# Kernel optimization log

Hardware: AMD Instinct MI355X
Metric: run time of the kernel (lower is better)

Reference implementation:

```python
import jax, jax.numpy as jnp
import numpy as np
from functools import partial

THRESH = 0.5   # similarity_threshold
EPS = 1e-8     # F.cosine_similarity eps


def setup_inputs() -> dict:
    key = jax.random.key(0)
    # uniform positive vectors -> pairwise cosine ~0.75 > threshold, so merges actually occur
    embeddings = jax.random.uniform(key, (8192, 512), dtype=jnp.float32)
    return {"embeddings": embeddings}


@partial(jax.jit, static_argnums=())
def _greedy_match(embs):
    """One merge round. Returns (partner[i] or -1, consumed-as-j flag per i).
    Faithful to the original greedy: scan i in order; i picks argmax-sim j>i among
    not-yet-merged with sim >= threshold; both get marked merged."""
    n = embs.shape[0]
    norms = jnp.maximum(jnp.linalg.norm(embs, axis=-1), EPS)
    sim = (embs @ embs.T) / (norms[:, None] * norms[None, :])  # [n, n]
    idx = jnp.arange(n)

    def step(merged, xs):
        i, row = xs
        was_consumed = merged[i]
        valid = (~merged) & (idx > i)
        scores = jnp.where(valid, row, -jnp.inf)
        j = jnp.argmax(scores)
        ok = (~was_consumed) & (scores[j] >= THRESH)
        merged = merged.at[i].set(was_consumed | ok)
        merged = merged.at[j].set(merged[j] | ok)
        return merged, (jnp.where(ok, j, -1), was_consumed)

    _, (partners, consumed) = jax.lax.scan(step, jnp.zeros(n, bool), (idx, sim))
    return partners, consumed


def reference(embeddings):
    embs = embeddings
    # outer while-loop mirrors the module: iterate rounds until no merge or n<=1
    while embs.shape[0] > 1:
        partners, consumed = _greedy_match(embs)
        partners_np = np.asarray(partners)
        if not (partners_np >= 0).any():  # merge_occurred == False
            break
        safe = jnp.maximum(partners, 0)
        # fuse_embeddings: clamp(v1 + v2, max=1.0); non-leaders keep their row
        fused = jnp.where((partners >= 0)[:, None],
                          jnp.minimum(embs + embs[safe], 1.0), embs)
        survivors = np.where(~np.asarray(consumed))[0]  # rows not consumed as a j
        embs = fused[survivors]
    return embs
```

## Files before the change

### kernel.cpp

```cpp
#include <hip/hip_runtime.h>
#include <math.h>

#define D 512
#define THRESH 0.5f
#define NMAX 8192
#define TOPK 64
#define INFI 0x7fffffff

typedef short bhalf8 __attribute__((ext_vector_type(8)));
typedef float f32x4 __attribute__((ext_vector_type(4)));

__device__ __forceinline__ unsigned long long rdl64(unsigned long long x, int l) {
    unsigned lo = (unsigned)__builtin_amdgcn_readlane((int)(unsigned)(x & 0xffffffffull), l);
    unsigned hi = (unsigned)__builtin_amdgcn_readlane((int)(unsigned)(x >> 32), l);
    return ((unsigned long long)hi << 32) | lo;
}

__global__ void k_init(int* dn, int n) { *dn = n; }

__global__ void k_prep(const float* __restrict__ E, float* __restrict__ norms,
                       unsigned short* __restrict__ H, const int* __restrict__ dn) {
    int n = *dn;
    int row = blockIdx.x;
    if (row >= n) return;
    int t = threadIdx.x;
    float4 v = ((const float4*)(E + (size_t)row * D))[t];
    float s = v.x * v.x + v.y * v.y + v.z * v.z + v.w * v.w;
    #pragma unroll
    for (int o = 32; o > 0; o >>= 1) s += __shfl_down(s, o, 64);
    __shared__ float ls[2];
    if ((t & 63) == 0) ls[t >> 6] = s;
    float f[4] = {v.x, v.y, v.z, v.w};
    unsigned short r[4];
    #pragma unroll
    for (int u = 0; u < 4; ++u) {
        unsigned int b = __float_as_uint(f[u]);
        r[u] = (unsigned short)((b + 0x7FFFu + ((b >> 16) & 1u)) >> 16);
    }
    uint2 packed;
    packed.x = (unsigned)r[0] | ((unsigned)r[1] << 16);
    packed.y = (unsigned)r[2] | ((unsigned)r[3] << 16);
    *(uint2*)(H + (size_t)row * D + t * 4) = packed;
    __syncthreads();
    if (t == 0) norms[row] = fmaxf(sqrtf(ls[0] + ls[1]), 1e-8f);
}

#define LDSTRIDE 72
__global__ void __launch_bounds__(256) k_mfma_sim(
    const unsigned short* __restrict__ H, const float* __restrict__ norms,
    float* __restrict__ sim, int tile_start, int TR, int simStride,
    const int* __restrict__ dn)
{
    int n = *dn;
    if (tile_start >= n) return;
    int row0 = tile_start + blockIdx.y * 128;
    int col0 = blockIdx.x * 128;
    if (row0 >= n || col0 >= n) return;
    if (col0 + 128 <= row0 + 1) return;

    __shared__ unsigned short As[128 * LDSTRIDE];
    __shared__ unsigned short Bs[128 * LDSTRIDE];
    int tid = threadIdx.x;
    int lane = tid & 63;
    int wave = tid >> 6;
    int wr = wave >> 1;
    int wc = wave & 1;
    int krow = lane & 15;
    int kgrp = (lane >> 4) * 8;

    f32x4 acc[4][4];
    #pragma unroll
    for (int m = 0; m < 4; ++m)
        #pragma unroll
        for (int t = 0; t < 4; ++t)
            acc[m][t] = (f32x4){0.f, 0.f, 0.f, 0.f};

    for (int k0 = 0; k0 < D; k0 += 64) {
        #pragma unroll
        for (int it = 0; it < 4; ++it) {
            int c  = tid + it * 256;
            int rr = c >> 3;
            int cc = c & 7;
            uint4 va = make_uint4(0, 0, 0, 0);
            int gra = row0 + rr;
            if (gra < n) va = *(const uint4*)(H + (size_t)gra * D + k0 + cc * 8);
            *(uint4*)&As[rr * LDSTRIDE + cc * 8] = va;
            uint4 vb = make_uint4(0, 0, 0, 0);
            int grb = col0 + rr;
            if (grb < n) vb = *(const uint4*)(H + (size_t)grb * D + k0 + cc * 8);
            *(uint4*)&Bs[rr * LDSTRIDE + cc * 8] = vb;
        }
        __syncthreads();
        #pragma unroll
        for (int kk = 0; kk < 64; kk += 32) {
            bhalf8 a[4], b[4];
            #pragma unroll
            for (int m = 0; m < 4; ++m)
                a[m] = *(const bhalf8*)&As[(wr * 64 + m * 16 + krow) * LDSTRIDE + kk + kgrp];
            #pragma unroll
            for (int t = 0; t < 4; ++t)
                b[t] = *(const bhalf8*)&Bs[(wc * 64 + t * 16 + krow) * LDSTRIDE + kk + kgrp];
            #pragma unroll
            for (int m = 0; m < 4; ++m)
                #pragma unroll
                for (int t = 0; t < 4; ++t)
                    acc[m][t] = __builtin_amdgcn_mfma_f32_16x16x32_bf16(a[m], b[t], acc[m][t], 0, 0, 0);
        }
        __syncthreads();
    }

    int fcol = lane & 15;
    int frow = (lane >> 4) * 4;
    #pragma unroll
    for (int m = 0; m < 4; ++m) {
        #pragma unroll
        for (int t = 0; t < 4; ++t) {
            #pragma unroll
            for (int v = 0; v < 4; ++v) {
                int gr = row0 + wr * 64 + m * 16 + frow + v;
                int gc = col0 + wc * 64 + t * 16 + fcol;
                if (gr < n && gc < n)
                    sim[(size_t)(gr - tile_start) * simStride + gc] =
                        acc[m][t][v] / (norms[gr] * norms[gc]);
            }
        }
    }
}

__global__ void __launch_bounds__(64) k_topk(
    const float* __restrict__ sim, int tile_start, int TR, int simStride,
    uint2* __restrict__ tkP, int* __restrict__ needFix,
    const int* __restrict__ dn)
{
    int n = *dn;
    int r = blockIdx.x;
    int i = tile_start + r;
    if (r >= TR || i >= n) return;
    int lane = threadIdx.x;
    const float* srow = sim + (size_t)r * simStride;

    float v[8]; int id[8];
    #pragma unroll
    for (int u = 0; u < 8; ++u) { v[u] = -INFINITY; id[u] = INFI; }
    float ovV = -INFINITY; int ovI = INFI;

    for (int j = i + 1 + lane; j < n; j += 64) {
        float x = srow[j];
        if (x > v[7] || (x == v[7] && j < id[7])) {
            if (v[7] > ovV || (v[7] == ovV && id[7] < ovI)) { ovV = v[7]; ovI = id[7]; }
            int p = 7;
            #pragma unroll
            for (int u = 6; u >= 0; --u) {
                bool mv = (x > v[u]) || (x == v[u] && j < id[u]);
                if (mv) { v[u + 1] = v[u]; id[u + 1] = id[u]; p = u; }
            }
            v[p] = x; id[p] = j;
        } else {
            if (x > ovV || (x == ovV && j < ovI)) { ovV = x; ovI = j; }
        }
    }

    int pos = 0;
    float myV = -INFINITY; int myI = INFI;
    for (int k = 0; k < TOPK; ++k) {
        float hv = (pos < 8) ? v[pos] : -INFINITY;
        int   hi = (pos < 8) ? id[pos] : INFI;
        float bv = hv; int bi = hi;
        #pragma unroll
        for (int o = 1; o < 64; o <<= 1) {
            float xv = __shfl_xor(bv, o, 64);
            int   xi = __shfl_xor(bi, o, 64);
            if (xv > bv || (xv == bv && xi < bi)) { bv = xv; bi = xi; }
        }
        if (pos < 8 && hv == bv && hi == bi) pos++;
        if (k == lane) { myV = bv; myI = bi; }
    }
    tkP[(size_t)i * TOPK + lane] = make_uint2(__float_as_uint(myV), (unsigned)myI);

    float v64 = __shfl(myV, 63, 64);
    int   i64 = __shfl(myI, 63, 64);
    float oV = ovV; int oI = ovI;
    #pragma unroll
    for (int o = 1; o < 64; o <<= 1) {
        float xv = __shfl_xor(oV, o, 64);
        int   xi = __shfl_xor(oI, o, 64);
        if (xv > oV || (xv == oV && xi < oI)) { oV = xv; oI = xi; }
    }
    int bad = (oV > v64) || (oV == v64 && oI < i64);
    if (lane == 0) needFix[i] = bad;
}

__global__ void __launch_bounds__(64) k_topkfix(
    const float* __restrict__ sim, int tile_start, int TR, int simStride,
    uint2* __restrict__ tkP, const int* __restrict__ needFix,
    const int* __restrict__ dn)
{
    int n = *dn;
    int r = blockIdx.x;
    int i = tile_start + r;
    if (r >= TR || i >= n) return;
    if (!needFix[i]) return;
    int lane = threadIdx.x;
    __shared__ float lv[64][TOPK];
    __shared__ int   li[64][TOPK];
    for (int u = 0; u < TOPK; ++u) { lv[lane][u] = -INFINITY; li[lane][u] = INFI; }
    const float* srow = sim + (size_t)r * simStride;
    for (int j = i + 1 + lane; j < n; j += 64) {
        float x = srow[j];
        float wv = lv[lane][TOPK - 1]; int wi = li[lane][TOPK - 1];
        if (x > wv || (x == wv && j < wi)) {
            int p = TOPK - 1;
            for (int u = TOPK - 2; u >= 0; --u) {
                float uv = lv[lane][u]; int ui = li[lane][u];
                if (x > uv || (x == uv && j < ui)) { lv[lane][u + 1] = uv; li[lane][u + 1] = ui; p = u; }
                else break;
            }
            lv[lane][p] = x; li[lane][p] = j;
        }
    }
    int pos = 0;
    float myV = -INFINITY; int myI = INFI;
    for (int k = 0; k < TOPK; ++k) {
        float hv = (pos < TOPK) ? lv[lane][pos] : -INFINITY;
        int   hi = (pos < TOPK) ? li[lane][pos] : INFI;
        float bv = hv; int bi = hi;
        #pragma unroll
        for (int o = 1; o < 64; o <<= 1) {
            float xv = __shfl_xor(bv, o, 64);
            int   xi = __shfl_xor(bi, o, 64);
            if (xv > bv || (xv == bv && xi < bi)) { bv = xv; bi = xi; }
        }
        if (pos < TOPK && hv == bv && hi == bi) pos++;
        if (k == lane) { myV = bv; myI = bi; }
    }
    tkP[(size_t)i * TOPK + lane] = make_uint2(__float_as_uint(myV), (unsigned)myI);
}

__device__ __attribute__((noinline)) void dot_fallback(
    int r, int n, int lane, const float* __restrict__ E,
    const float* __restrict__ norms, const unsigned long long* lmask,
    float& obv, int& obj)
{
    float ni = norms[r];
    float4 e0 = *(const float4*)(E + (size_t)r * D + lane * 8);
    float4 e1 = *(const float4*)(E + (size_t)r * D + lane * 8 + 4);
    float bbv = -INFINITY; int bbj = INFI;
    int w0 = (r + 1) >> 6, wN = (n + 63) >> 6;
    for (int ww = w0; ww < wN; ++ww) {
        unsigned long long um = ~lmask[ww];
        if (ww == (r >> 6)) um &= (~0ull) << ((r & 63) + 1);
        int over = (ww << 6) + 64 - n;
        if (over > 0) um &= (over >= 64) ? 0ull : ((~0ull) >> over);
        while (um) {
            int b = __builtin_ctzll(um);
            um &= um - 1;
            int jj = (ww << 6) + b;
            float4 a0 = *(const float4*)(E + (size_t)jj * D + lane * 8);
            float4 a1 = *(const float4*)(E + (size_t)jj * D + lane * 8 + 4);
            float s = e0.x * a0.x + e0.y * a0.y + e0.z * a0.z + e0.w * a0.w
                    + e1.x * a1.x + e1.y * a1.y + e1.z * a1.z + e1.w * a1.w;
            #pragma unroll
            for (int o = 1; o < 64; o <<= 1) s += __shfl_xor(s, o, 64);
            float sv = s / (ni * norms[jj]);
            if (sv > bbv || (sv == bbv && jj < bbj)) { bbv = sv; bbj = jj; }
        }
    }
    obv = bbv; obj = bbj;
}

__global__ void __launch_bounds__(64) k_scan7(
    const uint2* __restrict__ tkP,
    const float* __restrict__ E, const float* __restrict__ norms,
    const float* __restrict__ sim, int simStride, int simOk,
    int* __restrict__ partner, int* __restrict__ srcIdx,
    int* __restrict__ dn)
{
    int n = *dn;
    int lane = threadIdx.x;
    int base_ = lane << 7;

    __shared__ unsigned long long lmask[128];
    lmask[lane] = 0ull;
    lmask[64 + lane] = 0ull;
    asm volatile("s_waitcnt lgkmcnt(0)" ::: "memory");

    unsigned long long own0 = 0ull, own1 = 0ull;
    unsigned long long cm0 = 0ull, cm1 = 0ull;
    int nextStart = 0;
    unsigned skipA = 0, skipB = 0;
    const uint2 SENT = make_uint2(0xFF800000u, (unsigned)INFI);

#define WINDOW(U0, U1, LO) {                                                   \
    long long kw_ = (long long)(LO) - base_;                                   \
    if (kw_ > 0) {                                                             \
        if (kw_ >= 128) { U0 = 0ull; U1 = 0ull; }                              \
        else if (kw_ >= 64) { U0 = 0ull; if (kw_ > 64) U1 &= (~0ull) << (int)(kw_ - 64); } \
        else U0 &= (~0ull) << (int)kw_;                                        \
    }                                                                          \
    int kn_ = n - base_;                                                       \
    if (kn_ <= 0) { U0 = 0ull; U1 = 0ull; }                                    \
    else if (kn_ < 64) { U0 &= (~0ull) >> (64 - kn_); U1 = 0ull; }             \
    else if (kn_ < 128) { U1 = (kn_ == 64) ? 0ull : (U1 & ((~0ull) >> (128 - kn_))); } }

#define SETSEL(P, g, v) {                                                       \
    if ((g)==0) P##0=(v); else if ((g)==1) P##1=(v); else if ((g)==2) P##2=(v); \
    else if ((g)==3) P##3=(v); else if ((g)==4) P##4=(v); else if ((g)==5) P##5=(v); \
    else if ((g)==6) P##6=(v); else P##7=(v); }

#define BUILD(P, C, SK) do {                                                    \
    P##0=INFI;P##1=INFI;P##2=INFI;P##3=INFI;P##4=INFI;P##5=INFI;P##6=INFI;P##7=INFI; \
    SK = 0;                                                                     \
    unsigned long long u0_ = ~own0, u1_ = ~own1;                                \
    WINDOW(u0_, u1_, nextStart)                                                 \
    unsigned long long balv_ = __ballot((u0_ | u1_) != 0ull);                   \
    int got_ = 0, lastSel_ = -1;                                                \
    while (got_ < 8 && balv_) {                                                 \
        int L_ = (int)__builtin_ctzll(balv_); balv_ &= balv_ - 1;               \
        unsigned long long w0_ = rdl64(u0_, L_);                                \
        unsigned long long w1_ = rdl64(u1_, L_);                                \
        int bs_ = L_ << 7;                                                      \
        while (w0_ && got_ < 8) { int b_ = (int)__builtin_ctzll(w0_); w0_ &= w0_-1; \
            int v_ = bs_ + b_; lastSel_ = v_; SETSEL(P, got_, v_); got_++; }    \
        while (w1_ && got_ < 8) { int b_ = (int)__builtin_ctzll(w1_); w1_ &= w1_-1; \
            int v_ = bs_ + 64 + b_; lastSel_ = v_; SETSEL(P, got_, v_); got_++; } \
    }                                                                           \
    nextStart = (got_ > 0) ? (lastSel_ + 1) : n;                                \
    C##0 = (P##0 < n) ? tkP[(size_t)P##0 * TOPK + lane] : SENT;                 \
    C##1 = (P##1 < n) ? tkP[(size_t)P##1 * TOPK + lane] : SENT;                 \
    C##2 = (P##2 < n) ? tkP[(size_t)P##2 * TOPK + lane] : SENT;                 \
    C##3 = (P##3 < n) ? tkP[(size_t)P##3 * TOPK + lane] : SENT;                 \
    C##4 = (P##4 < n) ? tkP[(size_t)P##4 * TOPK + lane] : SENT;                 \
    C##5 = (P##5 < n) ? tkP[(size_t)P##5 * TOPK + lane] : SENT;                 \
    C##6 = (P##6 < n) ? tkP[(size_t)P##6 * TOPK + lane] : SENT;                 \
    C##7 = (P##7 < n) ? tkP[(size_t)P##7 * TOPK + lane] : SENT;                 \
} while (0)

#define SETBIT(v) { if (lane == ((v) >> 7)) {                                   \
    if (((v) >> 6) & 1) { own1 |= 1ull << ((v) & 63); lmask[2*lane+1] = own1; } \
    else                { own0 |= 1ull << ((v) & 63); lmask[2*lane]   = own0; } } }
#define SETCMB(v) { if (lane == ((v) >> 7)) {                                   \
    if (((v) >> 6) & 1) cm1 |= 1ull << ((v) & 63);                              \
    else                cm0 |= 1ull << ((v) & 63); } }

#define SKIPUPD(jv)                                                             \
    skipA |= ((jv==ra0)?1u:0)|((jv==ra1)?2u:0)|((jv==ra2)?4u:0)|((jv==ra3)?8u:0)   \
           |((jv==ra4)?16u:0)|((jv==ra5)?32u:0)|((jv==ra6)?64u:0)|((jv==ra7)?128u:0); \
    skipB |= ((jv==rb0)?1u:0)|((jv==rb1)?2u:0)|((jv==rb2)?4u:0)|((jv==rb3)?8u:0)   \
           |((jv==rb4)?16u:0)|((jv==rb5)?32u:0)|((jv==rb6)?64u:0)|((jv==rb7)?128u:0);

#define POPSLOT(k) if (ra##k != INFI && !((skipA >> k) & 1u)) {                 \
    int r_ = ra##k;                                                             \
    int ci_ = (int)ca##k.y;                                                     \
    bool okc_ = ci_ < n;                                                        \
    int wi_ = okc_ ? (ci_ >> 6) : 0;                                            \
    unsigned long long wm_ = *(volatile unsigned long long*)&lmask[wi_];        \
    bool valid_ = okc_ && !((wm_ >> (ci_ & 63)) & 1ull);                        \
    unsigned long long bal_ = __ballot(valid_);                                 \
    int j_ = -1; float v_ = -INFINITY;                                          \
    if (bal_) {                                                                 \
        int L_ = (int)__builtin_ctzll(bal_);                                    \
        j_ = __builtin_amdgcn_readlane(ci_, L_);                                \
        v_ = __uint_as_float((unsigned)__builtin_amdgcn_readlane((int)ca##k.x, L_)); \
    } else {                                                                    \
        unsigned long long u0_ = ~own0, u1_ = ~own1;                            \
        WINDOW(u0_, u1_, r_ + 1)                                                \
        if (__ballot((u0_ | u1_) != 0ull)) {                                    \
            if (simOk) {                                                        \
                const float* srow_ = sim + (size_t)r_ * simStride;              \
                float bv_ = -INFINITY; int bj_ = INFI;                          \
                for (int jb_ = (r_ + 1) & ~63; jb_ < n; jb_ += 64) {            \
                    int j2_ = jb_ + lane;                                       \
                    unsigned long long wm2_ = *(volatile unsigned long long*)&lmask[j2_ >> 6]; \
                    bool ok2_ = (j2_ > r_) && (j2_ < n) && !((wm2_ >> (j2_ & 63)) & 1ull); \
                    float v2_ = ok2_ ? srow_[j2_] : -INFINITY;                  \
                    int   i2_ = ok2_ ? j2_ : INFI;                              \
                    if (v2_ > bv_ || (v2_ == bv_ && i2_ < bj_)) { bv_ = v2_; bj_ = i2_; } \
                }                                                               \
                _Pragma("unroll")                                               \
                for (int o_ = 1; o_ < 64; o_ <<= 1) {                           \
                    float xv_ = __shfl_xor(bv_, o_, 64);                        \
                    int   xi_ = __shfl_xor(bj_, o_, 64);                        \
                    if (xv_ > bv_ || (xv_ == bv_ && xi_ < bj_)) { bv_ = xv_; bj_ = xi_; } \
                }                                                               \
                if (bj_ != INFI) { v_ = bv_; j_ = bj_; }                        \
            } else {                                                            \
                dot_fallback(r_, n, lane, E, norms, (const unsigned long long*)lmask, v_, j_); \
                if (j_ == INFI) j_ = -1;                                        \
            }                                                                   \
        }                                                                       \
    }                                                                           \
    bool ok_ = (j_ >= 0) && (v_ >= THRESH);                                     \
    if (ok_) {                                                                  \
        SETBIT(r_); SETBIT(j_); SETCMB(j_);                                     \
        asm volatile("s_waitcnt lgkmcnt(0)" ::: "memory");                      \
        SKIPUPD(j_)                                                             \
        if (lane == 0) partner[r_] = j_;                                        \
    } else {                                                                    \
        if (lane == 0) partner[r_] = -1;                                        \
    }                                                                           \
}

    int ra0,ra1,ra2,ra3,ra4,ra5,ra6,ra7;
    int rb0,rb1,rb2,rb3,rb4,rb5,rb6,rb7;
    uint2 ca0,ca1,ca2,ca3,ca4,ca5,ca6,ca7;
    uint2 cb0,cb1,cb2,cb3,cb4,cb5,cb6,cb7;

    BUILD(ra, ca, skipA);
    int guard = NMAX + 8;
    while (ra0 != INFI && guard-- > 0) {
        BUILD(rb, cb, skipB);
        POPSLOT(0) POPSLOT(1) POPSLOT(2) POPSLOT(3)
        POPSLOT(4) POPSLOT(5) POPSLOT(6) POPSLOT(7)
        ra0=rb0; ra1=rb1; ra2=rb2; ra3=rb3; ra4=rb4; ra5=rb5; ra6=rb6; ra7=rb7;
        ca0=cb0; ca1=cb1; ca2=cb2; ca3=cb3; ca4=cb4; ca5=cb5; ca6=cb6; ca7=cb7;
        skipA = skipB;
    }

    {
        int base = lane << 7;
        unsigned long long s0 = ~cm0, s1 = ~cm1;
        int kn = n - base;
        if (kn <= 0) { s0 = 0ull; s1 = 0ull; }
        else if (kn < 64) { s0 &= (~0ull) >> (64 - kn); s1 = 0ull; }
        else if (kn < 128) { s1 = (kn == 64) ? 0ull : (s1 & ((~0ull) >> (128 - kn))); }
        int cnt = __builtin_popcountll(s0) + __builtin_popcountll(s1);
        int inc = cnt;
        #pragma unroll
        for (int o = 1; o < 64; o <<= 1) {
            int t = __shfl_up(inc, o, 64);
            if (lane >= o) inc += t;
        }
        int p = inc - cnt;
        while (s0) { int b = __builtin_ctzll(s0); s0 &= s0 - 1; srcIdx[p++] = base + b; }
        while (s1) { int b = __builtin_ctzll(s1); s1 &= s1 - 1; srcIdx[p++] = base + 64 + b; }
        if (lane == 63) *dn = inc;
    }
#undef WINDOW
#undef SETSEL
#undef BUILD
#undef SETBIT
#undef SETCMB
#undef SKIPUPD
#undef POPSLOT
}

__global__ void k_fuse(const float* __restrict__ cur, float* __restrict__ nxt,
                       const int* __restrict__ srcIdx, const int* __restrict__ partner,
                       const int* __restrict__ dn) {
    int nn = *dn;
    int k = blockIdx.x;
    if (k >= nn) return;
    int t = threadIdx.x;
    int i = srcIdx[k];
    int p = partner[i];
    float4 v = ((const float4*)(cur + (size_t)i * D))[t];
    if (p >= 0) {
        float4 w = ((const float4*)(cur + (size_t)p * D))[t];
        v.x = fminf(v.x + w.x, 1.0f);
        v.y = fminf(v.y + w.y, 1.0f);
        v.z = fminf(v.z + w.z, 1.0f);
        v.w = fminf(v.w + w.w, 1.0f);
    }
    ((float4*)(nxt + (size_t)k * D))[t] = v;
}

__global__ void k_copyout(const float* __restrict__ src, float* __restrict__ dst, int nelem) {
    int i = blockIdx.x * 256 + threadIdx.x;
    if (i < nelem) dst[i] = src[i];
}

extern "C" void kernel_launch(void* const* d_in, const int* in_sizes, int n_in,
                              void* d_out, int out_size, void* d_ws, size_t ws_size,
                              hipStream_t stream) {
    const float* input = (const float*)d_in[0];
    const int N0 = in_sizes[0] / D;
    char* ws = (char*)d_ws;

    const size_t embA = (size_t)(N0 / 2) * D * sizeof(float);
    const size_t embB = (size_t)(N0 / 4) * D * sizeof(float);
    const size_t embH = (size_t)N0 * D * sizeof(unsigned short);
    float* bufA = (float*)ws;
    float* bufB = (float*)(ws + embA);
    unsigned short* curh = (unsigned short*)(ws + embA + embB);
    char* aux = ws + embA + embB + embH;
    float* norms   = (float*)(aux);
    int*   partner = (int*)(aux + 32 * 1024);
    int*   srcIdx  = (int*)(aux + 96 * 1024);
    int*   dn      = (int*)(aux + 128 * 1024);
    int*   needFix = (int*)(aux + 160 * 1024);
    uint2* tkP     = (uint2*)(aux + 256 * 1024);
    float* simTile = (float*)(aux + 256 * 1024 + (size_t)NMAX * TOPK * 8);
    const size_t fixedBytes = embA + embB + embH + 256 * 1024 + (size_t)NMAX * TOPK * 8;

    int TR = NMAX;
    while (TR > 128 && fixedBytes + (size_t)TR * N0 * sizeof(float) > ws_size) TR >>= 1;
    int simOk = (TR == N0) ? 1 : 0;

    const int ROUNDS = 16;
    k_init<<<1, 1, 0, stream>>>(dn, N0);
    for (int r = 0; r < ROUNDS; ++r) {
        const float* cur = (r == 0) ? input : ((r & 1) ? bufA : bufB);
        float* nxt = (r & 1) ? bufB : bufA;
        k_prep<<<N0, 128, 0, stream>>>(cur, norms, curh, dn);
        int NT = N0 / TR;
        for (int t = 0; t < NT; ++t) {
            dim3 g(N0 / 128, TR / 128);
            k_mfma_sim<<<g, 256, 0, stream>>>(curh, norms, simTile, t * TR, TR, N0, dn);
            k_topk<<<TR, 64, 0, stream>>>(simTile, t * TR, TR, N0, tkP, needFix, dn);
            k_topkfix<<<TR, 64, 0, stream>>>(simTile, t * TR, TR, N0, tkP, needFix, dn);
        }
        k_scan7<<<1, 64, 0, stream>>>(tkP, cur, norms, simTile, N0, simOk, partner, srcIdx, dn);
        k_fuse<<<N0, 128, 0, stream>>>(cur, nxt, srcIdx, partner, dn);
    }
    float* fin = bufB;
    k_copyout<<<(out_size + 255) / 256, 256, 0, stream>>>(fin, (float*)d_out, out_size);
}
```

Before: 16.35 ms.

## Batch 16 rows per scan step with precomputed validity ballots

The single-wavefront greedy scan now handles 16 unmerged rows per iteration instead of 8, packing row indices as 16-bit fields in four 64-bit registers. It computes the candidate validity ballots and row-active masks for the whole batch up front, then patches them incrementally when a merge consumes a later row or candidate. Initialising partner to -1 moves into k_prep, so the scan writes partner only for merged rows. The aim is to cut the serial latency of the sequential scan by exposing more independent loads and ballots per step, at the cost of more register pressure and extra per-merge patch work.

```diff
diff --git a/kernel.cpp b/kernel.cpp
--- a/kernel.cpp
+++ b/kernel.cpp
@@ -19,7 +19,8 @@
 __global__ void k_init(int* dn, int n) { *dn = n; }
 
 __global__ void k_prep(const float* __restrict__ E, float* __restrict__ norms,
-                       unsigned short* __restrict__ H, const int* __restrict__ dn) {
+                       unsigned short* __restrict__ H, int* __restrict__ partner,
+                       const int* __restrict__ dn) {
     int n = *dn;
     int row = blockIdx.x;
     if (row >= n) return;
@@ -41,6 +42,7 @@
     packed.x = (unsigned)r[0] | ((unsigned)r[1] << 16);
     packed.y = (unsigned)r[2] | ((unsigned)r[3] << 16);
     *(uint2*)(H + (size_t)row * D + t * 4) = packed;
+    if (t == 64) partner[row] = -1;
     __syncthreads();
     if (t == 0) norms[row] = fmaxf(sqrtf(ls[0] + ls[1]), 1e-8f);
 }
@@ -236,9 +238,32 @@
     tkP[(size_t)i * TOPK + lane] = make_uint2(__float_as_uint(myV), (unsigned)myI);
 }
 
+__device__ __attribute__((noinline)) void sim_fallback(
+    int r, int n, int lane, const float* __restrict__ sim, int simStride,
+    const volatile unsigned long long* lmask, float& obv, int& obj)
+{
+    const float* srow = sim + (size_t)r * simStride;
+    float bv = -INFINITY; int bj = INFI;
+    for (int jb = (r + 1) & ~63; jb < n; jb += 64) {
+        int j2 = jb + lane;
+        unsigned long long wm = lmask[j2 >> 6];
+        bool ok2 = (j2 > r) && (j2 < n) && !((wm >> (j2 & 63)) & 1ull);
+        float v2 = ok2 ? srow[j2] : -INFINITY;
+        int   i2 = ok2 ? j2 : INFI;
+        if (v2 > bv || (v2 == bv && i2 < bj)) { bv = v2; bj = i2; }
+    }
+    #pragma unroll
+    for (int o = 1; o < 64; o <<= 1) {
+        float xv = __shfl_xor(bv, o, 64);
+        int   xi = __shfl_xor(bj, o, 64);
+        if (xv > bv || (xv == bv && xi < bj)) { bv = xv; bj = xi; }
+    }
+    obv = bv; obj = bj;
+}
+
 __device__ __attribute__((noinline)) void dot_fallback(
     int r, int n, int lane, const float* __restrict__ E,
-    const float* __restrict__ norms, const unsigned long long* lmask,
+    const float* __restrict__ norms, const volatile unsigned long long* lmask,
     float& obv, int& obj)
 {
     float ni = norms[r];
@@ -268,7 +293,7 @@
     obv = bbv; obj = bbj;
 }
 
-__global__ void __launch_bounds__(64) k_scan7(
+__global__ void __launch_bounds__(64) k_scan8(
     const uint2* __restrict__ tkP,
     const float* __restrict__ E, const float* __restrict__ norms,
     const float* __restrict__ sim, int simStride, int simOk,
@@ -287,7 +312,6 @@
     unsigned long long own0 = 0ull, own1 = 0ull;
     unsigned long long cm0 = 0ull, cm1 = 0ull;
     int nextStart = 0;
-    unsigned skipA = 0, skipB = 0;
     const uint2 SENT = make_uint2(0xFF800000u, (unsigned)INFI);
 
 #define WINDOW(U0, U1, LO) {                                                   \
@@ -302,37 +326,38 @@
     else if (kn_ < 64) { U0 &= (~0ull) >> (64 - kn_); U1 = 0ull; }             \
     else if (kn_ < 128) { U1 = (kn_ == 64) ? 0ull : (U1 & ((~0ull) >> (128 - kn_))); } }
 
-#define SETSEL(P, g, v) {                                                       \
-    if ((g)==0) P##0=(v); else if ((g)==1) P##1=(v); else if ((g)==2) P##2=(v); \
-    else if ((g)==3) P##3=(v); else if ((g)==4) P##4=(v); else if ((g)==5) P##5=(v); \
-    else if ((g)==6) P##6=(v); else P##7=(v); }
-
-#define BUILD(P, C, SK) do {                                                    \
-    P##0=INFI;P##1=INFI;P##2=INFI;P##3=INFI;P##4=INFI;P##5=INFI;P##6=INFI;P##7=INFI; \
-    SK = 0;                                                                     \
+#define ROWP(R0, R1, R2, R3, m) ((int)((((m) < 4 ? (R0) : (m) < 8 ? (R1) : (m) < 12 ? (R2) : (R3)) >> (((m) & 3) * 16)) & 0xffffull))
+
+#define PUT16(R0, R1, R2, R3, g, v) {                                           \
+    unsigned long long vv_ = ((unsigned long long)(unsigned)(v)) << (((g) & 3) * 16); \
+    unsigned long long mm_ = 0xffffull << (((g) & 3) * 16);                     \
+    if ((g) < 4) R0 = (R0 & ~mm_) | vv_;                                        \
+    else if ((g) < 8) R1 = (R1 & ~mm_) | vv_;                                   \
+    else if ((g) < 12) R2 = (R2 & ~mm_) | vv_;                                  \
+    else R3 = (R3 & ~mm_) | vv_; }
+
+#define BUILD16(R0, R1, R2, R3, CAND) do {                                      \
+    R0 = ~0ull; R1 = ~0ull; R2 = ~0ull; R3 = ~0ull;                             \
     unsigned long long u0_ = ~own0, u1_ = ~own1;                                \
     WINDOW(u0_, u1_, nextStart)                                                 \
     unsigned long long balv_ = __ballot((u0_ | u1_) != 0ull);                   \
     int got_ = 0, lastSel_ = -1;                                                \
-    while (got_ < 8 && balv_) {                                                 \
+    while (got_ < 16 && balv_) {                                                \
         int L_ = (int)__builtin_ctzll(balv_); balv_ &= balv_ - 1;               \
         unsigned long long w0_ = rdl64(u0_, L_);                                \
         unsigned long long w1_ = rdl64(u1_, L_);                                \
         int bs_ = L_ << 7;                                                      \
-        while (w0_ && got_ < 8) { int b_ = (int)__builtin_ctzll(w0_); w0_ &= w0_-1; \
-            int v_ = bs_ + b_; lastSel_ = v_; SETSEL(P, got_, v_); got_++; }    \
-        while (w1_ && got_ < 8) { int b_ = (int)__builtin_ctzll(w1_); w1_ &= w1_-1; \
-            int v_ = bs_ + 64 + b_; lastSel_ = v_; SETSEL(P, got_, v_); got_++; } \
+        while (w0_ && got_ < 16) { int b_ = (int)__builtin_ctzll(w0_); w0_ &= w0_ - 1; \
+            int v_ = bs_ + b_; PUT16(R0, R1, R2, R3, got_, v_); lastSel_ = v_; got_++; } \
+        while (w1_ && got_ < 16) { int b_ = (int)__builtin_ctzll(w1_); w1_ &= w1_ - 1; \
+            int v_ = bs_ + 64 + b_; PUT16(R0, R1, R2, R3, got_, v_); lastSel_ = v_; got_++; } \
     }                                                                           \
     nextStart = (got_ > 0) ? (lastSel_ + 1) : n;                                \
-    C##0 = (P##0 < n) ? tkP[(size_t)P##0 * TOPK + lane] : SENT;                 \
-    C##1 = (P##1 < n) ? tkP[(size_t)P##1 * TOPK + lane] : SENT;                 \
-    C##2 = (P##2 < n) ? tkP[(size_t)P##2 * TOPK + lane] : SENT;                 \
-    C##3 = (P##3 < n) ? tkP[(size_t)P##3 * TOPK + lane] : SENT;                 \
-    C##4 = (P##4 < n) ? tkP[(size_t)P##4 * TOPK + lane] : SENT;                 \
-    C##5 = (P##5 < n) ? tkP[(size_t)P##5 * TOPK + lane] : SENT;                 \
-    C##6 = (P##6 < n) ? tkP[(size_t)P##6 * TOPK + lane] : SENT;                 \
-    C##7 = (P##7 < n) ? tkP[(size_t)P##7 * TOPK + lane] : SENT;                 \
+    _Pragma("unroll")                                                           \
+    for (int m_ = 0; m_ < 16; ++m_) {                                           \
+        int rm_ = ROWP(R0, R1, R2, R3, m_);                                     \
+        CAND[m_] = (rm_ < n) ? tkP[(size_t)rm_ * TOPK + lane] : SENT;           \
+    }                                                                           \
 } while (0)
 
 #define SETBIT(v) { if (lane == ((v) >> 7)) {                                   \
@@ -342,78 +367,67 @@
     if (((v) >> 6) & 1) cm1 |= 1ull << ((v) & 63);                              \
     else                cm0 |= 1ull << ((v) & 63); } }
 
-#define SKIPUPD(jv)                                                             \
-    skipA |= ((jv==ra0)?1u:0)|((jv==ra1)?2u:0)|((jv==ra2)?4u:0)|((jv==ra3)?8u:0)   \
-           |((jv==ra4)?16u:0)|((jv==ra5)?32u:0)|((jv==ra6)?64u:0)|((jv==ra7)?128u:0); \
-    skipB |= ((jv==rb0)?1u:0)|((jv==rb1)?2u:0)|((jv==rb2)?4u:0)|((jv==rb3)?8u:0)   \
-           |((jv==rb4)?16u:0)|((jv==rb5)?32u:0)|((jv==rb6)?64u:0)|((jv==rb7)?128u:0);
-
-#define POPSLOT(k) if (ra##k != INFI && !((skipA >> k) & 1u)) {                 \
-    int r_ = ra##k;                                                             \
-    int ci_ = (int)ca##k.y;                                                     \
-    bool okc_ = ci_ < n;                                                        \
-    int wi_ = okc_ ? (ci_ >> 6) : 0;                                            \
-    unsigned long long wm_ = *(volatile unsigned long long*)&lmask[wi_];        \
-    bool valid_ = okc_ && !((wm_ >> (ci_ & 63)) & 1ull);                        \
-    unsigned long long bal_ = __ballot(valid_);                                 \
-    int j_ = -1; float v_ = -INFINITY;                                          \
-    if (bal_) {                                                                 \
-        int L_ = (int)__builtin_ctzll(bal_);                                    \
-        j_ = __builtin_amdgcn_readlane(ci_, L_);                                \
-        v_ = __uint_as_float((unsigned)__builtin_amdgcn_readlane((int)ca##k.x, L_)); \
-    } else {                                                                    \
-        unsigned long long u0_ = ~own0, u1_ = ~own1;                            \
-        WINDOW(u0_, u1_, r_ + 1)                                                \
-        if (__ballot((u0_ | u1_) != 0ull)) {                                    \
-            if (simOk) {                                                        \
-                const float* srow_ = sim + (size_t)r_ * simStride;              \
-                float bv_ = -INFINITY; int bj_ = INFI;                          \
-                for (int jb_ = (r_ + 1) & ~63; jb_ < n; jb_ += 64) {            \
-                    int j2_ = jb_ + lane;                                       \
-                    unsigned long long wm2_ = *(volatile unsigned long long*)&lmask[j2_ >> 6]; \
-                    bool ok2_ = (j2_ > r_) && (j2_ < n) && !((wm2_ >> (j2_ & 63)) & 1ull); \
-                    float v2_ = ok2_ ? srow_[j2_] : -INFINITY;                  \
-                    int   i2_ = ok2_ ? j2_ : INFI;                              \
-                    if (v2_ > bv_ || (v2_ == bv_ && i2_ < bj_)) { bv_ = v2_; bj_ = i2_; } \
-                }                                                               \
-                _Pragma("unroll")                                               \
-                for (int o_ = 1; o_ < 64; o_ <<= 1) {                           \
-                    float xv_ = __shfl_xor(bv_, o_, 64);                        \
-                    int   xi_ = __shfl_xor(bj_, o_, 64);                        \
-                    if (xv_ > bv_ || (xv_ == bv_ && xi_ < bj_)) { bv_ = xv_; bj_ = xi_; } \
-                }                                                               \
-                if (bj_ != INFI) { v_ = bv_; j_ = bj_; }                        \
-            } else {                                                            \
-                dot_fallback(r_, n, lane, E, norms, (const unsigned long long*)lmask, v_, j_); \
-                if (j_ == INFI) j_ = -1;                                        \
-            }                                                                   \
-        }                                                                       \
-    }                                                                           \
-    bool ok_ = (j_ >= 0) && (v_ >= THRESH);                                     \
-    if (ok_) {                                                                  \
-        SETBIT(r_); SETBIT(j_); SETCMB(j_);                                     \
-        asm volatile("s_waitcnt lgkmcnt(0)" ::: "memory");                      \
-        SKIPUPD(j_)                                                             \
-        if (lane == 0) partner[r_] = j_;                                        \
-    } else {                                                                    \
-        if (lane == 0) partner[r_] = -1;                                        \
-    }                                                                           \
-}
-
-    int ra0,ra1,ra2,ra3,ra4,ra5,ra6,ra7;
-    int rb0,rb1,rb2,rb3,rb4,rb5,rb6,rb7;
-    uint2 ca0,ca1,ca2,ca3,ca4,ca5,ca6,ca7;
-    uint2 cb0,cb1,cb2,cb3,cb4,cb5,cb6,cb7;
-
-    BUILD(ra, ca, skipA);
+    unsigned long long rpA0, rpA1, rpA2, rpA3, rpB0, rpB1, rpB2, rpB3;
+    uint2 candA[16], candB[16];
+
+    BUILD16(rpA0, rpA1, rpA2, rpA3, candA);
     int guard = NMAX + 8;
-    while (ra0 != INFI && guard-- > 0) {
-        BUILD(rb, cb, skipB);
-        POPSLOT(0) POPSLOT(1) POPSLOT(2) POPSLOT(3)
-        POPSLOT(4) POPSLOT(5) POPSLOT(6) POPSLOT(7)
-        ra0=rb0; ra1=rb1; ra2=rb2; ra3=rb3; ra4=rb4; ra5=rb5; ra6=rb6; ra7=rb7;
-        ca0=cb0; ca1=cb1; ca2=cb2; ca3=cb3; ca4=cb4; ca5=cb5; ca6=cb6; ca7=cb7;
-        skipA = skipB;
+    while ((int)(rpA0 & 0xffffull) != 0xffff && guard-- > 0) {
+        asm volatile("s_waitcnt lgkmcnt(0)" ::: "memory");
+        unsigned act = 0;
+        #pragma unroll
+        for (int m = 0; m < 16; ++m) {
+            int rm = ROWP(rpA0, rpA1, rpA2, rpA3, m);
+            if (rm < n) {
+                unsigned long long w = *(volatile unsigned long long*)&lmask[rm >> 6];
+                if (!((w >> (rm & 63)) & 1ull)) act |= 1u << m;
+            }
+        }
+        unsigned long long ball[16];
+        #pragma unroll
+        for (int m = 0; m < 16; ++m) {
+            int ci = (int)candA[m].y;
+            bool okc = ci < n;
+            unsigned long long w = okc ? *(volatile unsigned long long*)&lmask[ci >> 6] : 0ull;
+            bool valid = okc && !((w >> (ci & 63)) & 1ull);
+            ball[m] = __ballot(valid);
+        }
+        BUILD16(rpB0, rpB1, rpB2, rpB3, candB);
+        #pragma unroll
+        for (int m = 0; m < 16; ++m) {
+            if (!((act >> m) & 1u)) continue;
+            int r_ = ROWP(rpA0, rpA1, rpA2, rpA3, m);
+            unsigned long long b_ = ball[m];
+            int j_ = -1; float v_ = -INFINITY;
+            if (b_) {
+                int L_ = (int)__builtin_ctzll(b_);
+                j_ = __builtin_amdgcn_readlane((int)candA[m].y, L_);
+                v_ = __uint_as_float((unsigned)__builtin_amdgcn_readlane((int)candA[m].x, L_));
+            } else {
+                unsigned long long u0_ = ~own0, u1_ = ~own1;
+                WINDOW(u0_, u1_, r_ + 1)
+                if (__ballot((u0_ | u1_) != 0ull)) {
+                    asm volatile("s_waitcnt lgkmcnt(0)" ::: "memory");
+                    if (simOk) sim_fallback(r_, n, lane, sim, simStride,
+                                            (const volatile unsigned long long*)lmask, v_, j_);
+                    else       dot_fallback(r_, n, lane, E, norms,
+                                            (const volatile unsigned long long*)lmask, v_, j_);
+                    if (j_ == INFI) j_ = -1;
+                }
+            }
+            if (j_ >= 0 && v_ >= THRESH) {
+                SETBIT(r_); SETBIT(j_); SETCMB(j_);
+                if (lane == 0) partner[r_] = j_;
+                #pragma unroll
+                for (int m2 = 0; m2 < 16; ++m2) if (m2 > m) {
+                    ball[m2] &= ~__ballot((int)candA[m2].y == j_);
+                    if (ROWP(rpA0, rpA1, rpA2, rpA3, m2) == j_) act &= ~(1u << m2);
+                }
+            }
+        }
+        rpA0 = rpB0; rpA1 = rpB1; rpA2 = rpB2; rpA3 = rpB3;
+        #pragma unroll
+        for (int m = 0; m < 16; ++m) candA[m] = candB[m];
     }
 
     {
@@ -436,12 +450,11 @@
         if (lane == 63) *dn = inc;
     }
 #undef WINDOW
-#undef SETSEL
-#undef BUILD
+#undef ROWP
+#undef PUT16
+#undef BUILD16
 #undef SETBIT
 #undef SETCMB
-#undef SKIPUPD
-#undef POPSLOT
 }
 
 __global__ void k_fuse(const float* __restrict__ cur, float* __restrict__ nxt,
@@ -501,7 +514,7 @@
     for (int r = 0; r < ROUNDS; ++r) {
         const float* cur = (r == 0) ? input : ((r & 1) ? bufA : bufB);
         float* nxt = (r & 1) ? bufB : bufA;
-        k_prep<<<N0, 128, 0, stream>>>(cur, norms, curh, dn);
+        k_prep<<<N0, 128, 0, stream>>>(cur, norms, curh, partner, dn);
         int NT = N0 / TR;
         for (int t = 0; t < NT; ++t) {
             dim3 g(N0 / 128, TR / 128);
@@ -509,7 +522,7 @@
             k_topk<<<TR, 64, 0, stream>>>(simTile, t * TR, TR, N0, tkP, needFix, dn);
             k_topkfix<<<TR, 64, 0, stream>>>(simTile, t * TR, TR, N0, tkP, needFix, dn);
         }
-        k_scan7<<<1, 64, 0, stream>>>(tkP, cur, norms, simTile, N0, simOk, partner, srcIdx, dn);
+        k_scan8<<<1, 64, 0, stream>>>(tkP, cur, norms, simTile, N0, simOk, partner, srcIdx, dn);
         k_fuse<<<N0, 128, 0, stream>>>(cur, nxt, srcIdx, partner, dn);
     }
     float* fin = bufB;
```

Result: faster. 15.61 ms (-4.5%).
